# Kernel tuning notes

Hardware: AMD Instinct MI355X
Metric: run time of the kernel (lower is better)

## Reference

```python
import jax, jax.numpy as jnp
import numpy as np
from jax import lax

N_HEAD, D_IN, D_HID, D_OUT = 8, 64, 64, 64
SEQ = 32768
STD = 1.0 / np.sqrt(D_HID * N_HEAD)


def _unif(key, shape):
    return jax.random.uniform(key, shape, jnp.float32, -STD, STD)


def setup_inputs() -> dict:
    key = jax.random.key(0)
    ks = jax.random.split(key, 12)
    D = N_HEAD * D_IN
    return {
        "inputs": jax.random.normal(ks[0], (SEQ, D), jnp.float32),
        "W_in": _unif(ks[1], (D, D)),
        "b_in": _unif(ks[2], (D,)),
        "W_gates": _unif(ks[3], (D_IN, 3 * D_HID)),
        "b_gates": _unif(ks[4], (3 * D_HID,)),
        "W_og": _unif(ks[5], (D_IN, D_HID)),
        "b_og": _unif(ks[6], (D_HID,)),
        "W_c": _unif(ks[7], (D_HID, D_OUT)),
        "b_c": _unif(ks[8], (D_OUT,)),
        "W_out": _unif(ks[9], (N_HEAD * D_OUT, N_HEAD * D_OUT)),
        "b_out": _unif(ks[10], (N_HEAD * D_OUT,)),
    }


def reference(inputs, W_in, b_in, W_gates, b_gates, W_og, b_og, W_c, b_c, W_out, b_out):
    S = inputs.shape[0]
    # input mixing across heads, then flatten: (S, H*d_in) -> (S*H, d_in)
    x = (inputs @ W_in + b_in).reshape(S * N_HEAD, D_IN)
    # FirstModule: fused gate projection
    g = x @ W_gates + b_gates  # (S*H, 3*d_hid)
    fg = jax.nn.sigmoid(g[:, :D_HID])
    ig = jax.nn.sigmoid(g[:, D_HID:2 * D_HID])
    h = jnp.tanh(g[:, 2 * D_HID:])
    hr = ig * h
    # linear recurrence c_t = fg_t * c_{t-1} + hr_t, c_0 = 0, via associative scan
    def comb(e1, e2):
        a1, b1 = e1
        a2, b2 = e2
        return (a1 * a2, b1 * a2 + b2)
    _, c = lax.associative_scan(comb, (fg, hr))  # (S*H, d_hid)
    # SecondModule: output gate and projection
    og = jax.nn.sigmoid(x @ W_og + b_og)
    o = (og * c) @ W_c + b_c  # (S*H, d_out)
    o = o.reshape(S, N_HEAD * D_OUT)
    return o @ W_out + b_out
```

## Files before the change

### kernel.cpp

```cpp
#include <hip/hip_runtime.h>


typedef unsigned short ushort;
typedef __bf16 bf16x8 __attribute__((ext_vector_type(8)));
typedef float f32x4 __attribute__((ext_vector_type(4)));

#define CROWS 64
#define NCH  4096
#define NSUP 64

#define GLOAD16(gp, lp) __builtin_amdgcn_global_load_lds( \
    (const __attribute__((address_space(1))) void*)(gp),  \
    (__attribute__((address_space(3))) void*)(lp), 16, 0, 0)

__device__ inline float b2f(ushort u) {
    return __builtin_bit_cast(float, (unsigned)u << 16);
}
__device__ inline ushort f2b(float f) {
    unsigned x = __builtin_bit_cast(unsigned, f);
    x += 0x7FFFu + ((x >> 16) & 1u);
    return (ushort)(x >> 16);
}
__device__ inline float sigm(float v) { return 1.0f / (1.0f + __expf(-v)); }
__device__ inline float tanh_fast(float v) { return 2.0f / (1.0f + __expf(-2.0f * v)) - 1.0f; }

__global__ void transpose512(const float* __restrict__ src, ushort* __restrict__ dst) {
    __shared__ float tile[32][33];
    const int tx = threadIdx.x & 31, ty = threadIdx.x >> 5;
    const int x0 = blockIdx.x * 32, y0 = blockIdx.y * 32;
    #pragma unroll
    for (int dy = 0; dy < 32; dy += 8)
        tile[ty + dy][tx] = src[(size_t)(y0 + ty + dy) * 512 + x0 + tx];
    __syncthreads();
    #pragma unroll
    for (int dy = 0; dy < 32; dy += 8)
        dst[(size_t)(x0 + ty + dy) * 512 + y0 + tx] = f2b(tile[tx][ty + dy]);
}

__global__ void prep_small(const float* __restrict__ W_gates, const float* __restrict__ W_og,
                           const float* __restrict__ W_c,
                           const float* __restrict__ b_gates, const float* __restrict__ b_og,
                           ushort* __restrict__ W2T, ushort* __restrict__ WcT, float* __restrict__ b2) {
    const int idx = blockIdx.x * 256 + threadIdx.x;
    if (idx < 16384) {
        const int n = idx >> 6, k = idx & 63;
        float v;
        if      (n < 64)  v = W_gates[k * 192 + 64 + n];
        else if (n < 128) v = W_gates[k * 192 + 128 + (n - 64)];
        else if (n < 192) v = W_gates[k * 192 + (n - 128)];
        else              v = W_og[k * 64 + (n - 192)];
        W2T[idx] = f2b(v);
    } else if (idx < 16384 + 4096) {
        const int i = idx - 16384;
        const int n = i >> 6, k = i & 63;
        WcT[i] = f2b(W_c[(k << 6) + n]);
    } else if (idx < 16384 + 4096 + 256) {
        const int i = idx - 20480;
        float v;
        if      (i < 64)  v = b_gates[64 + i];
        else if (i < 128) v = b_gates[128 + (i - 64)];
        else if (i < 192) v = b_gates[i - 128];
        else              v = b_og[i - 192];
        b2[i] = v;
    }
}

template <int BM, int BN, int WAVES_M, int WAVES_N, int A32, int C32>
__global__ __launch_bounds__(256)
void gemm_bt(const void* __restrict__ Av, const ushort* __restrict__ Bt,
             const float* __restrict__ bias, void* __restrict__ Cv,
             int M, int N, int K) {
    constexpr int WM = BM / WAVES_M, WN = BN / WAVES_N;
    constexpr int MT = WM / 16, NT = WN / 16;
    __shared__ __align__(16) ushort sA[BM * 32];
    __shared__ __align__(16) ushort sB[BN * 32];

    const int t = threadIdx.x, w = t >> 6, lane = t & 63;
    const int wm = (w / WAVES_N) * WM, wn = (w % WAVES_N) * WN;
    const long bm = (long)blockIdx.x * BM, bn = (long)blockIdx.y * BN;

    f32x4 acc[MT][NT] = {};

    for (int k0 = 0; k0 < K; k0 += 32) {
        if (A32) {
            const float* A = (const float*)Av;
            #pragma unroll
            for (int is = 0; is < BM / 32; ++is) {
                const int row = is * 32 + (t >> 3);
                const int cd = (t & 7) >> 1, half = t & 1;
                const float4 v = *(const float4*)(A + (bm + row) * (long)K + k0 + (t & 7) * 4);
                *(ushort4*)&sA[row * 32 + ((cd ^ (row & 3)) * 8) + half * 4] =
                    make_ushort4(f2b(v.x), f2b(v.y), f2b(v.z), f2b(v.w));
            }
        } else {
            const ushort* A = (const ushort*)Av;
            #pragma unroll
            for (int is = 0; is < BM / 64; ++is) {
                const int row = t >> 2, kc = t & 3;
                GLOAD16(A + (bm + is * 64 + row) * (long)K + k0 + ((kc ^ (row & 3)) * 8),
                        (char*)sA + is * 4096 + w * 1024);
            }
        }
        #pragma unroll
        for (int is = 0; is < BN / 64; ++is) {
            const int row = t >> 2, kc = t & 3;
            GLOAD16(Bt + (bn + is * 64 + row) * (long)K + k0 + ((kc ^ (row & 3)) * 8),
                    (char*)sB + is * 4096 + w * 1024);
        }
        __syncthreads();

        bf16x8 af[MT], bfr[NT];
        #pragma unroll
        for (int i = 0; i < MT; ++i) {
            const int row = wm + i * 16 + (lane & 15), c = lane >> 4;
            af[i] = *(const bf16x8*)&sA[row * 32 + ((c ^ (row & 3)) * 8)];
        }
        #pragma unroll
        for (int j = 0; j < NT; ++j) {
            const int rb = wn + j * 16 + (lane & 15), c = lane >> 4;
            bfr[j] = *(const bf16x8*)&sB[rb * 32 + ((c ^ (rb & 3)) * 8)];
        }
        #pragma unroll
        for (int i = 0; i < MT; ++i)
            #pragma unroll
            for (int j = 0; j < NT; ++j)
                acc[i][j] = __builtin_amdgcn_mfma_f32_16x16x32_bf16(af[i], bfr[j], acc[i][j], 0, 0, 0);
        __syncthreads();
    }

    #pragma unroll
    for (int i = 0; i < MT; ++i)
        #pragma unroll
        for (int j = 0; j < NT; ++j) {
            const long col = bn + wn + j * 16 + (lane & 15);
            const float bv = bias[col];
            #pragma unroll
            for (int r = 0; r < 4; ++r) {
                const long row = bm + wm + i * 16 + ((lane >> 4) << 2) + r;
                const float v = acc[i][j][r] + bv;
                if (C32) ((float*)Cv)[row * (long)N + col] = v;
                else     ((ushort*)Cv)[row * (long)N + col] = f2b(v);
            }
        }
}

template <int APPLY>
__global__ __launch_bounds__(256)
void gates_scan(const ushort* __restrict__ X, const ushort* __restrict__ W2T,
                const float* __restrict__ b2, const ushort* __restrict__ WcT,
                const float* __restrict__ b_c,
                float* __restrict__ Agg, float* __restrict__ Bgg,
                const float* __restrict__ PreS, ushort* __restrict__ O) {
    __shared__ __align__(16) char smem[40960];
    ushort* sA  = (ushort*)smem;
    ushort* sB  = (ushort*)(smem + 8192);
    ushort* sFG = (ushort*)smem;
    ushort* sHR = (ushort*)(smem + 9216);
    ushort* sOG = (ushort*)(smem + 18432);
    ushort* sP  = (ushort*)(smem + 27648);
    __shared__ __align__(16) ushort sWc[4096];

    const int t = threadIdx.x, w = t >> 6, lane = t & 63;
    const int blk = blockIdx.x;
    const long row0 = (long)blk * CROWS;

    {
        const int row = t >> 3, kc = t & 7;
        #pragma unroll
        for (int is = 0; is < 2; ++is)
            GLOAD16(X + (row0 + is * 32 + row) * 64 + ((kc ^ (row & 7)) * 8),
                    (char*)sA + is * 4096 + w * 1024);
        #pragma unroll
        for (int is = 0; is < 8; ++is)
            GLOAD16(W2T + (is * 32 + row) * 64 + ((kc ^ (row & 7)) * 8),
                    (char*)sB + is * 4096 + w * 1024);
        if (APPLY) {
            #pragma unroll
            for (int is = 0; is < 2; ++is)
                GLOAD16(WcT + (is * 32 + row) * 64 + ((kc ^ (row & 7)) * 8),
                        (char*)sWc + is * 4096 + w * 1024);
        }
    }
    __syncthreads();

    const int wm = (w >> 1) * 32;
    const int grpB = w & 1;
    const int colbase = grpB * 128;
    f32x4 acc[2][8] = {};
    #pragma unroll
    for (int kk = 0; kk < 2; ++kk) {
        bf16x8 af[2];
        #pragma unroll
        for (int i = 0; i < 2; ++i) {
            const int row = wm + i * 16 + (lane & 15), c = kk * 4 + (lane >> 4);
            af[i] = *(const bf16x8*)&sA[row * 64 + ((c ^ (row & 7)) * 8)];
        }
        #pragma unroll
        for (int j = 0; j < 8; ++j) {
            const int rb = colbase + j * 16 + (lane & 15), c = kk * 4 + (lane >> 4);
            const bf16x8 bf = *(const bf16x8*)&sB[rb * 64 + ((c ^ (rb & 7)) * 8)];
            #pragma unroll
            for (int i = 0; i < 2; ++i)
                acc[i][j] = __builtin_amdgcn_mfma_f32_16x16x32_bf16(af[i], bf, acc[i][j], 0, 0, 0);
        }
    }
    __syncthreads();

    if (!grpB) {
        #pragma unroll
        for (int jj = 0; jj < 4; ++jj) {
            const int ch = jj * 16 + (lane & 15);
            const float bi = b2[ch], bh = b2[64 + ch];
            #pragma unroll
            for (int i = 0; i < 2; ++i)
                #pragma unroll
                for (int r = 0; r < 4; ++r) {
                    const int row = wm + i * 16 + ((lane >> 4) << 2) + r;
                    const float gi = acc[i][jj][r] + bi;
                    const float gh = acc[i][jj + 4][r] + bh;
                    sHR[row * 72 + ch] = f2b(sigm(gi) * tanh_fast(gh));
                }
        }
    } else {
        #pragma unroll
        for (int jj = 0; jj < 4; ++jj) {
            const int ch = jj * 16 + (lane & 15);
            const float bfg = b2[128 + ch], bog = b2[192 + ch];
            #pragma unroll
            for (int i = 0; i < 2; ++i)
                #pragma unroll
                for (int r = 0; r < 4; ++r) {
                    const int row = wm + i * 16 + ((lane >> 4) << 2) + r;
                    sFG[row * 72 + ch] = f2b(sigm(acc[i][jj][r] + bfg));
                    if (APPLY) sOG[row * 72 + ch] = f2b(sigm(acc[i][jj + 4][r] + bog));
                }
        }
    }
    __syncthreads();

    if (!APPLY) {
        if (t < 64) {
            float a = 1.0f, b = 0.0f;
            #pragma unroll 8
            for (int r = 0; r < CROWS; ++r) {
                const float fg = b2f(sFG[r * 72 + t]);
                const float hr = b2f(sHR[r * 72 + t]);
                a *= fg;
                b = fmaf(b, fg, hr);
            }
            Agg[blk * 64 + t] = a;
            Bgg[blk * 64 + t] = b;
        }
        return;
    }

    if (t < 64) {
        float c = fmaf(PreS[(blk >> 6) * 64 + t], Agg[blk * 64 + t], Bgg[blk * 64 + t]);
        const int cch = t >> 3, half = t & 7;
        #pragma unroll 8
        for (int r = 0; r < CROWS; ++r) {
            const float fg = b2f(sFG[r * 72 + t]);
            const float hr = b2f(sHR[r * 72 + t]);
            c = fmaf(c, fg, hr);
            sP[r * 64 + ((cch ^ (r & 7)) * 8) + half] = f2b(b2f(sOG[r * 72 + t]) * c);
        }
    }
    __syncthreads();

    const int wm2 = (w >> 1) * 32, wn2 = (w & 1) * 32;
    f32x4 acc2[2][2] = {};
    #pragma unroll
    for (int kk = 0; kk < 2; ++kk) {
        bf16x8 pa[2], wb[2];
        #pragma unroll
        for (int i = 0; i < 2; ++i) {
            const int row = wm2 + i * 16 + (lane & 15), c = kk * 4 + (lane >> 4);
            pa[i] = *(const bf16x8*)&sP[row * 64 + ((c ^ (row & 7)) * 8)];
        }
        #pragma unroll
        for (int j = 0; j < 2; ++j) {
            const int rb = wn2 + j * 16 + (lane & 15), c = kk * 4 + (lane >> 4);
            wb[j] = *(const bf16x8*)&sWc[rb * 64 + ((c ^ (rb & 7)) * 8)];
        }
        #pragma unroll
        for (int i = 0; i < 2; ++i)
            #pragma unroll
            for (int j = 0; j < 2; ++j)
                acc2[i][j] = __builtin_amdgcn_mfma_f32_16x16x32_bf16(pa[i], wb[j], acc2[i][j], 0, 0, 0);
    }
    #pragma unroll
    for (int i = 0; i < 2; ++i)
        #pragma unroll
        for (int j = 0; j < 2; ++j) {
            const int col = wn2 + j * 16 + (lane & 15);
            const float bv = b_c[col];
            #pragma unroll
            for (int r = 0; r < 4; ++r) {
                const int row = wm2 + i * 16 + ((lane >> 4) << 2) + r;
                O[(row0 + row) * 64 + col] = f2b(acc2[i][j][r] + bv);
            }
        }
}

__global__ void scan_super(float* __restrict__ Agg, float* __restrict__ Bgg,
                           float* __restrict__ SA, float* __restrict__ SB) {
    const int s = blockIdx.x, ch = threadIdx.x;
    float a = 1.0f, b = 0.0f;
    #pragma unroll 8
    for (int j = 0; j < 64; ++j) {
        const int idx = (s * 64 + j) * 64 + ch;
        const float a2 = Agg[idx], bb = Bgg[idx];
        Agg[idx] = a;
        Bgg[idx] = b;
        a *= a2;
        b = fmaf(b, a2, bb);
    }
    SA[s * 64 + ch] = a;
    SB[s * 64 + ch] = b;
}

__global__ void scan_top(const float* __restrict__ SA, const float* __restrict__ SB,
                         float* __restrict__ PreS) {
    const int ch = threadIdx.x;
    float c = 0.0f;
    #pragma unroll 8
    for (int s = 0; s < 64; ++s) {
        PreS[s * 64 + ch] = c;
        c = fmaf(c, SA[s * 64 + ch], SB[s * 64 + ch]);
    }
}

extern "C" void kernel_launch(void* const* d_in, const int* in_sizes, int n_in,
                              void* d_out, int out_size, void* d_ws, size_t ws_size,
                              hipStream_t stream) {
    const float* inputs  = (const float*)d_in[0];
    const float* W_in    = (const float*)d_in[1];
    const float* b_in    = (const float*)d_in[2];
    const float* W_gates = (const float*)d_in[3];
    const float* b_gates = (const float*)d_in[4];
    const float* W_og    = (const float*)d_in[5];
    const float* b_og    = (const float*)d_in[6];
    const float* W_c     = (const float*)d_in[7];
    const float* b_c     = (const float*)d_in[8];
    const float* W_out   = (const float*)d_in[9];
    const float* b_out   = (const float*)d_in[10];
    float* out = (float*)d_out;

    char* ws = (char*)d_ws;
    ushort* X     = (ushort*)(ws);
    ushort* WinT  = (ushort*)(ws + 33554432);
    ushort* WoutT = (ushort*)(ws + 34078720);
    ushort* W2T   = (ushort*)(ws + 34603008);
    ushort* WcT   = (ushort*)(ws + 34635776);
    float*  b2    = (float*)(ws + 34643968);
    float*  Agg   = (float*)(ws + 34644992);
    float*  Bgg   = (float*)(ws + 35693568);
    float*  SA    = (float*)(ws + 36742144);
    float*  SB    = (float*)(ws + 36758528);
    float*  PreS  = (float*)(ws + 36774912);
    ushort* O = X;

    transpose512<<<dim3(16, 16), 256, 0, stream>>>(W_in, WinT);
    transpose512<<<dim3(16, 16), 256, 0, stream>>>(W_out, WoutT);
    prep_small<<<81, 256, 0, stream>>>(W_gates, W_og, W_c, b_gates, b_og, W2T, WcT, b2);

    gemm_bt<128, 128, 2, 2, 1, 0><<<dim3(256, 4), 256, 0, stream>>>(
        inputs, WinT, b_in, X, 32768, 512, 512);

    gates_scan<0><<<NCH, 256, 0, stream>>>(X, W2T, b2, WcT, b_c, Agg, Bgg, PreS, O);
    scan_super<<<NSUP, 64, 0, stream>>>(Agg, Bgg, SA, SB);
    scan_top<<<1, 64, 0, stream>>>(SA, SB, PreS);
    gates_scan<1><<<NCH, 256, 0, stream>>>(X, W2T, b2, WcT, b_c, Agg, Bgg, PreS, O);

    gemm_bt<128, 128, 2, 2, 0, 1><<<dim3(256, 4), 256, 0, stream>>>(
        O, WoutT, b_out, out, 32768, 512, 512);
}
```

Baseline: 324.6 us.

## Pre-convert inputs to bf16, load gates_scan operands directly from global, raise occupancy

When the workspace is large enough, the fp32 input is first converted to bf16 by a separate kernel, so the first GEMM reads bf16 instead of converting fp32 tiles inline. In gates_scan the LDS staging of X, W2T and WcT is dropped: MFMA fragments are loaded straight from global memory, which removes a barrier and shrinks shared memory so launch_bounds can request 4 blocks per CU. Sigmoid and tanh now use the hardware reciprocal instead of a division. The cost is an extra pass over the input, repeated uncoalesced global reads of the weights, and slightly less accurate activations.

```diff
diff --git a/kernel.cpp b/kernel.cpp
--- a/kernel.cpp
+++ b/kernel.cpp
@@ -21,8 +21,13 @@
     x += 0x7FFFu + ((x >> 16) & 1u);
     return (ushort)(x >> 16);
 }
-__device__ inline float sigm(float v) { return 1.0f / (1.0f + __expf(-v)); }
-__device__ inline float tanh_fast(float v) { return 2.0f / (1.0f + __expf(-2.0f * v)) - 1.0f; }
+__device__ inline float sigm(float v) { return __builtin_amdgcn_rcpf(1.0f + __expf(-v)); }
+__device__ inline float tanh_fast(float v) {
+    return 2.0f * __builtin_amdgcn_rcpf(1.0f + __expf(-2.0f * v)) - 1.0f;
+}
+__device__ inline f32x4 MFMA(bf16x8 a, bf16x8 b, f32x4 c) {
+    return __builtin_amdgcn_mfma_f32_16x16x32_bf16(a, b, c, 0, 0, 0);
+}
 
 __global__ void transpose512(const float* __restrict__ src, ushort* __restrict__ dst) {
     __shared__ float tile[32][33];
@@ -65,6 +70,15 @@
     }
 }
 
+__global__ __launch_bounds__(256)
+void cvt_f32_bf16(const float* __restrict__ src, ushort* __restrict__ dst) {
+    const long i = ((long)blockIdx.x * 256 + threadIdx.x) * 8;
+    const float4 v0 = *(const float4*)(src + i);
+    const float4 v1 = *(const float4*)(src + i + 4);
+    *(ushort4*)(dst + i)     = make_ushort4(f2b(v0.x), f2b(v0.y), f2b(v0.z), f2b(v0.w));
+    *(ushort4*)(dst + i + 4) = make_ushort4(f2b(v1.x), f2b(v1.y), f2b(v1.z), f2b(v1.w));
+}
+
 template <int BM, int BN, int WAVES_M, int WAVES_N, int A32, int C32>
 __global__ __launch_bounds__(256)
 void gemm_bt(const void* __restrict__ Av, const ushort* __restrict__ Bt,
@@ -124,7 +138,7 @@
         for (int i = 0; i < MT; ++i)
             #pragma unroll
             for (int j = 0; j < NT; ++j)
-                acc[i][j] = __builtin_amdgcn_mfma_f32_16x16x32_bf16(af[i], bfr[j], acc[i][j], 0, 0, 0);
+                acc[i][j] = MFMA(af[i], bfr[j], acc[i][j]);
         __syncthreads();
     }
 
@@ -145,77 +159,54 @@
 }
 
 template <int APPLY>
-__global__ __launch_bounds__(256)
+__global__ __launch_bounds__(256, 4)
 void gates_scan(const ushort* __restrict__ X, const ushort* __restrict__ W2T,
                 const float* __restrict__ b2, const ushort* __restrict__ WcT,
                 const float* __restrict__ b_c,
                 float* __restrict__ Agg, float* __restrict__ Bgg,
                 const float* __restrict__ PreS, ushort* __restrict__ O) {
-    __shared__ __align__(16) char smem[40960];
-    ushort* sA  = (ushort*)smem;
-    ushort* sB  = (ushort*)(smem + 8192);
+    __shared__ __align__(16) char smem[APPLY ? 35840 : 18432];
     ushort* sFG = (ushort*)smem;
     ushort* sHR = (ushort*)(smem + 9216);
     ushort* sOG = (ushort*)(smem + 18432);
     ushort* sP  = (ushort*)(smem + 27648);
-    __shared__ __align__(16) ushort sWc[4096];
 
     const int t = threadIdx.x, w = t >> 6, lane = t & 63;
     const int blk = blockIdx.x;
     const long row0 = (long)blk * CROWS;
 
-    {
-        const int row = t >> 3, kc = t & 7;
-        #pragma unroll
-        for (int is = 0; is < 2; ++is)
-            GLOAD16(X + (row0 + is * 32 + row) * 64 + ((kc ^ (row & 7)) * 8),
-                    (char*)sA + is * 4096 + w * 1024);
-        #pragma unroll
-        for (int is = 0; is < 8; ++is)
-            GLOAD16(W2T + (is * 32 + row) * 64 + ((kc ^ (row & 7)) * 8),
-                    (char*)sB + is * 4096 + w * 1024);
-        if (APPLY) {
-            #pragma unroll
-            for (int is = 0; is < 2; ++is)
-                GLOAD16(WcT + (is * 32 + row) * 64 + ((kc ^ (row & 7)) * 8),
-                        (char*)sWc + is * 4096 + w * 1024);
-        }
-    }
-    __syncthreads();
-
     const int wm = (w >> 1) * 32;
     const int grpB = w & 1;
     const int colbase = grpB * 128;
+    const int lr = lane & 15, lc = lane >> 4;
+
+    bf16x8 af[2][2];
+    #pragma unroll
+    for (int kk = 0; kk < 2; ++kk)
+        #pragma unroll
+        for (int i = 0; i < 2; ++i)
+            af[kk][i] = *(const bf16x8*)(X + (row0 + wm + i * 16 + lr) * 64 + kk * 32 + lc * 8);
+
     f32x4 acc[2][8] = {};
     #pragma unroll
-    for (int kk = 0; kk < 2; ++kk) {
-        bf16x8 af[2];
-        #pragma unroll
-        for (int i = 0; i < 2; ++i) {
-            const int row = wm + i * 16 + (lane & 15), c = kk * 4 + (lane >> 4);
-            af[i] = *(const bf16x8*)&sA[row * 64 + ((c ^ (row & 7)) * 8)];
-        }
+    for (int kk = 0; kk < 2; ++kk)
         #pragma unroll
         for (int j = 0; j < 8; ++j) {
-            const int rb = colbase + j * 16 + (lane & 15), c = kk * 4 + (lane >> 4);
-            const bf16x8 bf = *(const bf16x8*)&sB[rb * 64 + ((c ^ (rb & 7)) * 8)];
-            #pragma unroll
-            for (int i = 0; i < 2; ++i)
-                acc[i][j] = __builtin_amdgcn_mfma_f32_16x16x32_bf16(af[i], bf, acc[i][j], 0, 0, 0);
-        }
-    }
-    __syncthreads();
+            const bf16x8 bf = *(const bf16x8*)(W2T + (colbase + j * 16 + lr) * 64 + kk * 32 + lc * 8);
+            acc[0][j] = MFMA(af[kk][0], bf, acc[0][j]);
+            acc[1][j] = MFMA(af[kk][1], bf, acc[1][j]);
+        }
 
     if (!grpB) {
         #pragma unroll
         for (int jj = 0; jj < 4; ++jj) {
-            const int ch = jj * 16 + (lane & 15);
+            const int ch = jj * 16 + lr;
             const float bi = b2[ch], bh = b2[64 + ch];
             #pragma unroll
             for (int i = 0; i < 2; ++i)
                 #pragma unroll
                 for (int r = 0; r < 4; ++r) {
-                    const int row = wm + i * 16 + ((lane >> 4) << 2) + r;
+                    const int row = wm + i * 16 + (lc << 2) + r;
                     const float gi = acc[i][jj][r] + bi;
                     const float gh = acc[i][jj + 4][r] + bh;
                     sHR[row * 72 + ch] = f2b(sigm(gi) * tanh_fast(gh));
@@ -224,13 +215,13 @@
     } else {
         #pragma unroll
         for (int jj = 0; jj < 4; ++jj) {
-            const int ch = jj * 16 + (lane & 15);
+            const int ch = jj * 16 + lr;
             const float bfg = b2[128 + ch], bog = b2[192 + ch];
             #pragma unroll
             for (int i = 0; i < 2; ++i)
                 #pragma unroll
                 for (int r = 0; r < 4; ++r) {
-                    const int row = wm + i * 16 + ((lane >> 4) << 2) + r;
+                    const int row = wm + i * 16 + (lc << 2) + r;
                     sFG[row * 72 + ch] = f2b(sigm(acc[i][jj][r] + bfg));
                     if (APPLY) sOG[row * 72 + ch] = f2b(sigm(acc[i][jj + 4][r] + bog));
                 }
@@ -267,36 +258,34 @@
     }
     __syncthreads();
 
-    const int wm2 = (w >> 1) * 32, wn2 = (w & 1) * 32;
+    const int wn2 = grpB * 32;
     f32x4 acc2[2][2] = {};
     #pragma unroll
     for (int kk = 0; kk < 2; ++kk) {
         bf16x8 pa[2], wb[2];
         #pragma unroll
         for (int i = 0; i < 2; ++i) {
-            const int row = wm2 + i * 16 + (lane & 15), c = kk * 4 + (lane >> 4);
+            const int row = wm + i * 16 + lr, c = kk * 4 + lc;
             pa[i] = *(const bf16x8*)&sP[row * 64 + ((c ^ (row & 7)) * 8)];
         }
         #pragma unroll
+        for (int j = 0; j < 2; ++j)
+            wb[j] = *(const bf16x8*)(WcT + (wn2 + j * 16 + lr) * 64 + kk * 32 + lc * 8);
+        #pragma unroll
+        for (int i = 0; i < 2; ++i)
+            #pragma unroll
+            for (int j = 0; j < 2; ++j)
+                acc2[i][j] = MFMA(pa[i], wb[j], acc2[i][j]);
+    }
+    #pragma unroll
+    for (int i = 0; i < 2; ++i)
+        #pragma unroll
         for (int j = 0; j < 2; ++j) {
-            const int rb = wn2 + j * 16 + (lane & 15), c = kk * 4 + (lane >> 4);
-            wb[j] = *(const bf16x8*)&sWc[rb * 64 + ((c ^ (rb & 7)) * 8)];
-        }
-        #pragma unroll
-        for (int i = 0; i < 2; ++i)
-            #pragma unroll
-            for (int j = 0; j < 2; ++j)
-                acc2[i][j] = __builtin_amdgcn_mfma_f32_16x16x32_bf16(pa[i], wb[j], acc2[i][j], 0, 0, 0);
-    }
-    #pragma unroll
-    for (int i = 0; i < 2; ++i)
-        #pragma unroll
-        for (int j = 0; j < 2; ++j) {
-            const int col = wn2 + j * 16 + (lane & 15);
+            const int col = wn2 + j * 16 + lr;
             const float bv = b_c[col];
             #pragma unroll
             for (int r = 0; r < 4; ++r) {
-                const int row = wm2 + i * 16 + ((lane >> 4) << 2) + r;
+                const int row = wm + i * 16 + (lc << 2) + r;
                 O[(row0 + row) * 64 + col] = f2b(acc2[i][j][r] + bv);
             }
         }
@@ -358,14 +347,22 @@
     float*  SA    = (float*)(ws + 36742144);
     float*  SB    = (float*)(ws + 36758528);
     float*  PreS  = (float*)(ws + 36774912);
+    ushort* Ibf   = (ushort*)(ws + 36791296);
     ushort* O = X;
+    const bool big_ws = ws_size >= (36791296ull + 33554432ull);
 
     transpose512<<<dim3(16, 16), 256, 0, stream>>>(W_in, WinT);
     transpose512<<<dim3(16, 16), 256, 0, stream>>>(W_out, WoutT);
     prep_small<<<81, 256, 0, stream>>>(W_gates, W_og, W_c, b_gates, b_og, W2T, WcT, b2);
 
-    gemm_bt<128, 128, 2, 2, 1, 0><<<dim3(256, 4), 256, 0, stream>>>(
-        inputs, WinT, b_in, X, 32768, 512, 512);
+    if (big_ws) {
+        cvt_f32_bf16<<<8192, 256, 0, stream>>>(inputs, Ibf);
+        gemm_bt<128, 128, 2, 2, 0, 0><<<dim3(256, 4), 256, 0, stream>>>(
+            Ibf, WinT, b_in, X, 32768, 512, 512);
+    } else {
+        gemm_bt<128, 128, 2, 2, 1, 0><<<dim3(256, 4), 256, 0, stream>>>(
+            inputs, WinT, b_in, X, 32768, 512, 512);
+    }
 
     gates_scan<0><<<NCH, 256, 0, stream>>>(X, W2T, b2, WcT, b_c, Agg, Bgg, PreS, O);
     scan_super<<<NSUP, 64, 0, stream>>>(Agg, Bgg, SA, SB);
```

Result: no change. 318.3 us (-1.9%).
